# Kernel tuning notes

Hardware: AMD Instinct MI355X
Metric: run time of the kernel (lower is better)

Reference implementation:

```python
import jax, jax.numpy as jnp
import numpy as np

N_NODES = 100000
N_EDGES = 1000000
IN_FEAT = 128
OUT_FEAT = 128
NUM_RELS = 64
NUM_BASES = 16
SUBMAT_IN = IN_FEAT // NUM_BASES   # 8
SUBMAT_OUT = OUT_FEAT // NUM_BASES # 8


def setup_inputs() -> dict:
    key = jax.random.key(0)
    k = jax.random.split(key, 8)
    h = jax.random.normal(k[0], (N_NODES, IN_FEAT), dtype=jnp.float32)
    norm = jax.random.uniform(k[1], (N_EDGES, 1), dtype=jnp.float32)
    src = jax.random.randint(k[2], (N_EDGES,), 0, N_NODES, dtype=jnp.int32)
    dst = jax.random.randint(k[3], (N_EDGES,), 0, N_NODES, dtype=jnp.int32)
    r = jax.random.randint(k[4], (N_EDGES,), 0, NUM_RELS, dtype=jnp.int32)
    # learned params (xavier-uniform style scale)
    wscale = np.sqrt(6.0 / (SUBMAT_IN + SUBMAT_OUT)) * np.sqrt(2.0)
    weight = jax.random.uniform(k[5], (NUM_RELS, NUM_BASES * SUBMAT_IN * SUBMAT_OUT),
                                minval=-wscale, maxval=wscale, dtype=jnp.float32)
    lscale = np.sqrt(6.0 / (IN_FEAT + OUT_FEAT)) * np.sqrt(2.0)
    loop_weight = jax.random.uniform(k[6], (IN_FEAT, OUT_FEAT),
                                     minval=-lscale, maxval=lscale, dtype=jnp.float32)
    h_bias = jnp.zeros((OUT_FEAT,), dtype=jnp.float32)
    return {"h": h, "norm": norm, "weight": weight, "loop_weight": loop_weight,
            "h_bias": h_bias, "src": src, "dst": dst, "r": r}


def reference(h, norm, weight, loop_weight, h_bias, src, dst, r):
    E = src.shape[0]
    # per-edge block-diagonal weights: (E, B, si, so)
    w = weight[r].reshape(E, NUM_BASES, SUBMAT_IN, SUBMAT_OUT)
    # src features split into blocks: (E, B, si)
    hs = h[src].reshape(E, NUM_BASES, SUBMAT_IN)
    # small bmm per block, flatten to (E, OUT_FEAT)
    msg = jnp.einsum('ebi,ebio->ebo', hs, w).reshape(E, OUT_FEAT)
    msg = msg * norm
    # scatter-sum to destination nodes
    agg = jax.ops.segment_sum(msg, dst, num_segments=N_NODES)
    # self-loop message (dropout=0.0) + bias
    out = agg + h_bias + h @ loop_weight
    return jax.nn.relu(out)
```

## Files before the change

kernel.cpp:

```cpp
#include <hip/hip_runtime.h>
#include <stdint.h>

#define N_NODES 100000
#define N_EDGES 1000000
#define IN_F 128
#define OUT_F 128
#define NUM_RELS 64
#define NB_SCAN ((N_NODES + 255) / 256)
#define N_WAVES 16384

typedef _Float16 half2v __attribute__((ext_vector_type(2)));

__device__ __forceinline__ float dot2f(uint32_t hu, uint32_t wu, float acc) {
#if __has_builtin(__builtin_amdgcn_fdot2)
    return __builtin_amdgcn_fdot2(__builtin_bit_cast(half2v, hu),
                                  __builtin_bit_cast(half2v, wu), acc, false);
#else
    half2v a = __builtin_bit_cast(half2v, hu);
    half2v b = __builtin_bit_cast(half2v, wu);
    acc = fmaf((float)a.x, (float)b.x, acc);
    acc = fmaf((float)a.y, (float)b.y, acc);
    return acc;
#endif
}

__device__ __forceinline__ uint32_t pkh2(float x, float y) {
    half2v v;
    v.x = (_Float16)x;
    v.y = (_Float16)y;
    return __builtin_bit_cast(uint32_t, v);
}

__global__ __launch_bounds__(256) void gemm_selfloop(
    const float* __restrict__ h, const float* __restrict__ W,
    const float* __restrict__ bias, float* __restrict__ out, int n_nodes)
{
    const int tid = threadIdx.x;
    const int ty = tid >> 4, tx = tid & 15;
    const int node0 = blockIdx.x * 128 + ty * 8;
    const int o0 = tx * 8;

    float acc[8][8];
#pragma unroll
    for (int j = 0; j < 8; ++j)
#pragma unroll
        for (int i = 0; i < 8; ++i) acc[j][i] = 0.f;

    int nidx[8];
#pragma unroll
    for (int j = 0; j < 8; ++j) {
        int n = node0 + j;
        nidx[j] = n < n_nodes ? n : (n_nodes - 1);
    }

    for (int k = 0; k < IN_F; k += 4) {
        float hsv[8][4];
#pragma unroll
        for (int j = 0; j < 8; ++j) {
            float4 hv = *reinterpret_cast<const float4*>(h + (size_t)nidx[j] * IN_F + k);
            *reinterpret_cast<float4*>(hsv[j]) = hv;
        }
#pragma unroll
        for (int kk = 0; kk < 4; ++kk) {
            const float* wrow = W + (size_t)(k + kk) * OUT_F + o0;
            float wr[8];
            *reinterpret_cast<float4*>(wr)     = *reinterpret_cast<const float4*>(wrow);
            *reinterpret_cast<float4*>(wr + 4) = *reinterpret_cast<const float4*>(wrow + 4);
#pragma unroll
            for (int j = 0; j < 8; ++j) {
                const float hk = hsv[j][kk];
#pragma unroll
                for (int i = 0; i < 8; ++i)
                    acc[j][i] = fmaf(hk, wr[i], acc[j][i]);
            }
        }
    }

    float br[8];
    *reinterpret_cast<float4*>(br)     = *reinterpret_cast<const float4*>(bias + o0);
    *reinterpret_cast<float4*>(br + 4) = *reinterpret_cast<const float4*>(bias + o0 + 4);

#pragma unroll
    for (int j = 0; j < 8; ++j) {
        int n = node0 + j;
        if (n < n_nodes) {
            float4 v0, v1;
            v0.x = acc[j][0] + br[0]; v0.y = acc[j][1] + br[1];
            v0.z = acc[j][2] + br[2]; v0.w = acc[j][3] + br[3];
            v1.x = acc[j][4] + br[4]; v1.y = acc[j][5] + br[5];
            v1.z = acc[j][6] + br[6]; v1.w = acc[j][7] + br[7];
            float* op = out + (size_t)n * OUT_F + o0;
            *reinterpret_cast<float4*>(op)     = v0;
            *reinterpret_cast<float4*>(op + 4) = v1;
        }
    }
}

__global__ __launch_bounds__(256) void prep_hist_h16(
    const float* __restrict__ weight, uint32_t* __restrict__ wsw,
    const int* __restrict__ dst, int* __restrict__ cnt,
    const float* __restrict__ h, uint4* __restrict__ h16_4,
    int n_edges, int do_h16)
{
    int t = blockIdx.x * 256 + threadIdx.x;
    if (t < NUM_RELS * 512) {
        int r    = t >> 9;
        int p    = t & 511;
        int half = p >> 8;
        int w8   = p & 255;
        int l    = w8 >> 2;
        int ip   = w8 & 3;
        int b    = l >> 2;
        int q    = l & 3;
        int o    = 2 * q + half;
        const float* s = weight + (size_t)r * 1024 + b * 64 + (2 * ip) * 8 + o;
        half2v v;
        v.x = (_Float16)s[0];
        v.y = (_Float16)s[8];
        wsw[t] = __builtin_bit_cast(uint32_t, v);
        return;
    }
    int e = t - NUM_RELS * 512;
    if (e < n_edges) {
        atomicAdd(&cnt[dst[e]], 1);
        return;
    }
    if (!do_h16) return;
    int t2 = e - n_edges;
    if (t2 < N_NODES * IN_F / 8) {
        const float4* hp = reinterpret_cast<const float4*>(h + (size_t)t2 * 8);
        float4 a = hp[0], c = hp[1];
        uint4 r;
        r.x = pkh2(a.x, a.y);
        r.y = pkh2(a.z, a.w);
        r.z = pkh2(c.x, c.y);
        r.w = pkh2(c.z, c.w);
        h16_4[t2] = r;
    }
}

__global__ __launch_bounds__(256) void block_sums(
    const int* __restrict__ cnt, int* __restrict__ part, int n)
{
    __shared__ int sdata[256];
    int i = blockIdx.x * 256 + threadIdx.x;
    sdata[threadIdx.x] = (i < n) ? cnt[i] : 0;
    __syncthreads();
    for (int s = 128; s > 0; s >>= 1) {
        if (threadIdx.x < s) sdata[threadIdx.x] += sdata[threadIdx.x + s];
        __syncthreads();
    }
    if (threadIdx.x == 0) part[blockIdx.x] = sdata[0];
}

__global__ __launch_bounds__(256) void write_off2(
    const int* __restrict__ cnt, const int* __restrict__ part,
    int* __restrict__ off, int* __restrict__ cur, int n, int n_edges)
{
    __shared__ int sdata[256];
    __shared__ int buf[256];
    const int tid = threadIdx.x;
    const int bid = blockIdx.x;

    int psum = 0;
    for (int t = tid; t < bid; t += 256) psum += part[t];
    sdata[tid] = psum;
    __syncthreads();
    for (int s = 128; s > 0; s >>= 1) {
        if (tid < s) sdata[tid] += sdata[tid + s];
        __syncthreads();
    }
    const int blockoff = sdata[0];

    int i = bid * 256 + tid;
    int v = (i < n) ? cnt[i] : 0;
    buf[tid] = v;
    __syncthreads();
    for (int ofs = 1; ofs < 256; ofs <<= 1) {
        int t = (tid >= ofs) ? buf[tid - ofs] : 0;
        __syncthreads();
        buf[tid] += t;
        __syncthreads();
    }
    int excl = buf[tid] - v + blockoff;
    if (i < n) { off[i] = excl; cur[i] = excl; }
    if (i == n - 1) off[n] = n_edges;
}

__global__ __launch_bounds__(256) void fill_and_part(
    const int* __restrict__ src, const int* __restrict__ dst,
    const int* __restrict__ rel, const float* __restrict__ norm,
    int* __restrict__ cur, int2* __restrict__ emeta,
    const int* __restrict__ off, int* __restrict__ wstart, int n_edges)
{
    int t = blockIdx.x * 256 + threadIdx.x;
    if (t < n_edges) {
        int d = dst[t];
        int p = atomicAdd(&cur[d], 1);
        int2 m;
        m.x = src[t] | (rel[t] << 20);
        m.y = __float_as_int(norm[t]);
        emeta[p] = m;
    } else {
        int w = t - n_edges;
        if (w <= N_WAVES) {
            if (w == 0) {
                wstart[0] = 0;
            } else if (w == N_WAVES) {
                wstart[N_WAVES] = N_NODES;
            } else {
                int target = (int)(((long long)N_EDGES * w) / N_WAVES);
                int lo = 0, hi = N_NODES - 1;
                while (lo < hi) {
                    int mid = (lo + hi) >> 1;
                    if (off[mid + 1] > target) hi = mid; else lo = mid + 1;
                }
                wstart[w] = lo;
            }
        }
    }
}

__global__ __launch_bounds__(1024, 4) void gather_nodes9(
    const uint4* __restrict__ h16_4, const uint32_t* __restrict__ wsw,
    const int* __restrict__ off, const int2* __restrict__ emeta,
    const int* __restrict__ wstart, float* __restrict__ out)
{
    __shared__ uint32_t wlds[NUM_RELS * 512];

    {
        uint4* l4 = reinterpret_cast<uint4*>(wlds);
        const uint4* g4 = reinterpret_cast<const uint4*>(wsw);
        int t = threadIdx.x;
#pragma unroll
        for (int k = 0; k < 8; ++k)
            l4[t + k * 1024] = g4[t + k * 1024];
    }
    __syncthreads();

    const int lane = threadIdx.x & 63;
    const int wid  = threadIdx.x >> 6;
    const int wv   = blockIdx.x * 16 + wid;
    const int b = lane >> 2;
    const int q = lane & 3;
    const uint32_t lbase = (uint32_t)(lane * 4);

    const int n0 = wstart[wv];
    const int n1 = wstart[wv + 1];
    if (n0 >= n1) return;

    int j = off[n0];
    int e_next = off[n0 + 1];

    int2 m0 = emeta[j];
    int2 m1 = emeta[j + 1];
    int2 m2 = emeta[j + 2];
    uint4 hv0 = h16_4[((uint32_t)m0.x & 0xFFFFFu) * 16 + b];
    uint4 hv1 = h16_4[((uint32_t)m1.x & 0xFFFFFu) * 16 + b];

    uint32_t base0 = ((uint32_t)m0.x >> 20) * 512 + lbase;
    uint4 wa = *reinterpret_cast<const uint4*>(&wlds[base0]);
    uint4 wb = *reinterpret_cast<const uint4*>(&wlds[base0 + 256]);

    for (int d = n0; d < n1; ++d) {
        const int idx2 = (d + 2 < n1) ? d + 2 : n1;
        const int e_nn = off[idx2];
        float a0 = 0.f, a1 = 0.f;

        while (j < e_next) {
            int2 m3 = emeta[j + 3];
            uint4 hv2 = h16_4[((uint32_t)m2.x & 0xFFFFFu) * 16 + b];
            uint32_t bn = ((uint32_t)m1.x >> 20) * 512 + lbase;
            uint4 wna = *reinterpret_cast<const uint4*>(&wlds[bn]);
            uint4 wnb = *reinterpret_cast<const uint4*>(&wlds[bn + 256]);

            float s0 = dot2f(hv0.x, wa.x, 0.f);
            s0 = dot2f(hv0.y, wa.y, s0);
            s0 = dot2f(hv0.z, wa.z, s0);
            s0 = dot2f(hv0.w, wa.w, s0);
            float s1 = dot2f(hv0.x, wb.x, 0.f);
            s1 = dot2f(hv0.y, wb.y, s1);
            s1 = dot2f(hv0.z, wb.z, s1);
            s1 = dot2f(hv0.w, wb.w, s1);

            const float nm = __int_as_float(m0.y);
            a0 = fmaf(s0, nm, a0);
            a1 = fmaf(s1, nm, a1);

            m0 = m1; m1 = m2; m2 = m3;
            hv0 = hv1; hv1 = hv2;
            wa = wna; wb = wnb;
            ++j;
        }

        float2* op = reinterpret_cast<float2*>(out + (size_t)d * OUT_F + b * 8 + 2 * q);
        float2 bse = *op;
        float2 res;
        res.x = fmaxf(bse.x + a0, 0.f);
        res.y = fmaxf(bse.y + a1, 0.f);
        *op = res;

        e_next = e_nn;
    }
}

__global__ __launch_bounds__(1024, 4) void gather_nodes6(
    const float* __restrict__ h, const uint32_t* __restrict__ wsw,
    const int* __restrict__ off, const int2* __restrict__ emeta,
    const int* __restrict__ wstart, float* __restrict__ out)
{
    __shared__ uint32_t wlds[NUM_RELS * 512];
    {
        uint4* l4 = reinterpret_cast<uint4*>(wlds);
        const uint4* g4 = reinterpret_cast<const uint4*>(wsw);
        int t = threadIdx.x;
#pragma unroll
        for (int k = 0; k < 8; ++k)
            l4[t + k * 1024] = g4[t + k * 1024];
    }
    __syncthreads();

    const int lane = threadIdx.x & 63;
    const int wid  = threadIdx.x >> 6;
    const int wv   = blockIdx.x * 16 + wid;
    const int b = lane >> 2;
    const int q = lane & 3;
    const uint32_t lbase = (uint32_t)(lane * 4);

    const int n0 = wstart[wv];
    const int n1 = wstart[wv + 1];
    if (n0 >= n1) return;

    int j = off[n0];
    int2 m0 = emeta[j];
    int2 m1 = emeta[j + 1];
    int2 m2 = emeta[j + 2];

    const float4* hr0 = reinterpret_cast<const float4*>(
        h + (size_t)((uint32_t)m0.x & 0xFFFFFu) * IN_F + b * 8);
    float4 h0A = hr0[0], h0B = hr0[1];
    const float4* hr1 = reinterpret_cast<const float4*>(
        h + (size_t)((uint32_t)m1.x & 0xFFFFFu) * IN_F + b * 8);
    float4 h1A = hr1[0], h1B = hr1[1];

    uint32_t base0 = ((uint32_t)m0.x >> 20) * 512 + lbase;
    uint4 wa = *reinterpret_cast<const uint4*>(&wlds[base0]);
    uint4 wb = *reinterpret_cast<const uint4*>(&wlds[base0 + 256]);

    for (int d = n0; d < n1; ++d) {
        const int end_d = off[d + 1];
        float a0 = 0.f, a1 = 0.f;

        while (j < end_d) {
            int2 m3 = emeta[j + 3];
            const float4* hr2 = reinterpret_cast<const float4*>(
                h + (size_t)((uint32_t)m2.x & 0xFFFFFu) * IN_F + b * 8);
            float4 h2A = hr2[0], h2B = hr2[1];
            uint32_t bn = ((uint32_t)m1.x >> 20) * 512 + lbase;
            uint4 wna = *reinterpret_cast<const uint4*>(&wlds[bn]);
            uint4 wnb = *reinterpret_cast<const uint4*>(&wlds[bn + 256]);

            uint32_t h01 = __builtin_bit_cast(uint32_t, __builtin_amdgcn_cvt_pkrtz(h0A.x, h0A.y));
            uint32_t h23 = __builtin_bit_cast(uint32_t, __builtin_amdgcn_cvt_pkrtz(h0A.z, h0A.w));
            uint32_t h45 = __builtin_bit_cast(uint32_t, __builtin_amdgcn_cvt_pkrtz(h0B.x, h0B.y));
            uint32_t h67 = __builtin_bit_cast(uint32_t, __builtin_amdgcn_cvt_pkrtz(h0B.z, h0B.w));

            float s0 = dot2f(h01, wa.x, 0.f);
            s0 = dot2f(h23, wa.y, s0);
            s0 = dot2f(h45, wa.z, s0);
            s0 = dot2f(h67, wa.w, s0);
            float s1 = dot2f(h01, wb.x, 0.f);
            s1 = dot2f(h23, wb.y, s1);
            s1 = dot2f(h45, wb.z, s1);
            s1 = dot2f(h67, wb.w, s1);

            const float nm = __int_as_float(m0.y);
            a0 = fmaf(s0, nm, a0);
            a1 = fmaf(s1, nm, a1);

            m0 = m1; m1 = m2; m2 = m3;
            h0A = h1A; h0B = h1B; h1A = h2A; h1B = h2B;
            wa = wna; wb = wnb;
            ++j;
        }

        float2* op = reinterpret_cast<float2*>(out + (size_t)d * OUT_F + b * 8 + 2 * q);
        float2 bse = *op;
        float2 res;
        res.x = fmaxf(bse.x + a0, 0.f);
        res.y = fmaxf(bse.y + a1, 0.f);
        *op = res;
    }
}

extern "C" void kernel_launch(void* const* d_in, const int* in_sizes, int n_in,
                              void* d_out, int out_size, void* d_ws, size_t ws_size,
                              hipStream_t stream)
{
    const float* h      = (const float*)d_in[0];
    const float* norm   = (const float*)d_in[1];
    const float* weight = (const float*)d_in[2];
    const float* loop_w = (const float*)d_in[3];
    const float* bias   = (const float*)d_in[4];
    const int*   src    = (const int*)d_in[5];
    const int*   dst    = (const int*)d_in[6];
    const int*   rel    = (const int*)d_in[7];
    float* out = (float*)d_out;

    char* wsb = (char*)d_ws;
    char* ws0 = wsb;
    int*  cnt    = (int*)wsb;  wsb += sizeof(int) * N_NODES;
    int*  off    = (int*)wsb;  wsb += sizeof(int) * (N_NODES + 1);
    int*  cur    = (int*)wsb;  wsb += sizeof(int) * N_NODES;
    int*  part   = (int*)wsb;  wsb += sizeof(int) * 512;
    int*  wstart = (int*)wsb;  wsb += sizeof(int) * (N_WAVES + 1);
    wsb = (char*)(((uintptr_t)wsb + 15) & ~(uintptr_t)15);
    uint32_t* wsw = (uint32_t*)wsb; wsb += sizeof(uint32_t) * NUM_RELS * 512;
    int2* emeta = (int2*)wsb;  wsb += sizeof(int2) * (N_EDGES + 3);
    wsb = (char*)(((uintptr_t)wsb + 15) & ~(uintptr_t)15);
    uint4* h16_4 = (uint4*)wsb; wsb += (size_t)N_NODES * IN_F * 2;

    const int use_h16 = (size_t)(wsb - ws0) <= ws_size;

    hipMemsetAsync(cnt, 0, sizeof(int) * N_NODES, stream);
    hipMemsetAsync(emeta + N_EDGES, 0, 3 * sizeof(int2), stream);

    const int h16_threads = use_h16 ? (N_NODES * IN_F / 8) : 0;
    const int ph_grid = (NUM_RELS * 512 + N_EDGES + h16_threads + 255) / 256;
    prep_hist_h16<<<ph_grid, 256, 0, stream>>>(weight, wsw, dst, cnt,
                                               h, h16_4, N_EDGES, use_h16);
    block_sums<<<NB_SCAN, 256, 0, stream>>>(cnt, part, N_NODES);
    write_off2<<<NB_SCAN, 256, 0, stream>>>(cnt, part, off, cur, N_NODES, N_EDGES);
    const int fp_grid = (N_EDGES + N_WAVES + 1 + 255) / 256;
    fill_and_part<<<fp_grid, 256, 0, stream>>>(src, dst, rel, norm, cur, emeta,
                                               off, wstart, N_EDGES);

    gemm_selfloop<<<(N_NODES + 127) / 128, 256, 0, stream>>>(h, loop_w, bias, out, N_NODES);
    if (use_h16) {
        gather_nodes9<<<1024, 1024, 0, stream>>>(h16_4, wsw, off, emeta, wstart, out);
    } else {
        gather_nodes6<<<1024, 1024, 0, stream>>>(h, wsw, off, emeta, wstart, out);
    }
}
```

Measured before the change: 330.8 us.

## Fuse self-loop GEMM into prep kernel and make gather persistent with fewer blocks

```diff
diff --git a/kernel.cpp b/kernel.cpp
--- a/kernel.cpp
+++ b/kernel.cpp
@@ -8,6 +8,8 @@
 #define NUM_RELS 64
 #define NB_SCAN ((N_NODES + 255) / 256)
 #define N_WAVES 16384
+#define GEMM_B ((N_NODES + 127) / 128)
+#define GATHER_B 256
 
 typedef _Float16 half2v __attribute__((ext_vector_type(2)));
 
@@ -31,78 +33,77 @@
     return __builtin_bit_cast(uint32_t, v);
 }
 
-__global__ __launch_bounds__(256) void gemm_selfloop(
+__global__ __launch_bounds__(256) void prep_gemm_fused(
     const float* __restrict__ h, const float* __restrict__ W,
-    const float* __restrict__ bias, float* __restrict__ out, int n_nodes)
-{
-    const int tid = threadIdx.x;
-    const int ty = tid >> 4, tx = tid & 15;
-    const int node0 = blockIdx.x * 128 + ty * 8;
-    const int o0 = tx * 8;
-
-    float acc[8][8];
-#pragma unroll
-    for (int j = 0; j < 8; ++j)
-#pragma unroll
-        for (int i = 0; i < 8; ++i) acc[j][i] = 0.f;
-
-    int nidx[8];
-#pragma unroll
-    for (int j = 0; j < 8; ++j) {
-        int n = node0 + j;
-        nidx[j] = n < n_nodes ? n : (n_nodes - 1);
-    }
-
-    for (int k = 0; k < IN_F; k += 4) {
-        float hsv[8][4];
-#pragma unroll
-        for (int j = 0; j < 8; ++j) {
-            float4 hv = *reinterpret_cast<const float4*>(h + (size_t)nidx[j] * IN_F + k);
-            *reinterpret_cast<float4*>(hsv[j]) = hv;
-        }
-#pragma unroll
-        for (int kk = 0; kk < 4; ++kk) {
-            const float* wrow = W + (size_t)(k + kk) * OUT_F + o0;
-            float wr[8];
-            *reinterpret_cast<float4*>(wr)     = *reinterpret_cast<const float4*>(wrow);
-            *reinterpret_cast<float4*>(wr + 4) = *reinterpret_cast<const float4*>(wrow + 4);
-#pragma unroll
-            for (int j = 0; j < 8; ++j) {
-                const float hk = hsv[j][kk];
-#pragma unroll
-                for (int i = 0; i < 8; ++i)
-                    acc[j][i] = fmaf(hk, wr[i], acc[j][i]);
-            }
-        }
-    }
-
-    float br[8];
-    *reinterpret_cast<float4*>(br)     = *reinterpret_cast<const float4*>(bias + o0);
-    *reinterpret_cast<float4*>(br + 4) = *reinterpret_cast<const float4*>(bias + o0 + 4);
-
-#pragma unroll
-    for (int j = 0; j < 8; ++j) {
-        int n = node0 + j;
-        if (n < n_nodes) {
-            float4 v0, v1;
-            v0.x = acc[j][0] + br[0]; v0.y = acc[j][1] + br[1];
-            v0.z = acc[j][2] + br[2]; v0.w = acc[j][3] + br[3];
-            v1.x = acc[j][4] + br[4]; v1.y = acc[j][5] + br[5];
-            v1.z = acc[j][6] + br[6]; v1.w = acc[j][7] + br[7];
-            float* op = out + (size_t)n * OUT_F + o0;
-            *reinterpret_cast<float4*>(op)     = v0;
-            *reinterpret_cast<float4*>(op + 4) = v1;
-        }
-    }
-}
-
-__global__ __launch_bounds__(256) void prep_hist_h16(
+    const float* __restrict__ bias, float* __restrict__ out,
     const float* __restrict__ weight, uint32_t* __restrict__ wsw,
     const int* __restrict__ dst, int* __restrict__ cnt,
-    const float* __restrict__ h, uint4* __restrict__ h16_4,
-    int n_edges, int do_h16)
-{
-    int t = blockIdx.x * 256 + threadIdx.x;
+    uint4* __restrict__ h16_4, int n_edges, int do_h16)
+{
+    if (blockIdx.x < GEMM_B) {
+        const int tid = threadIdx.x;
+        const int ty = tid >> 4, tx = tid & 15;
+        const int node0 = blockIdx.x * 128 + ty * 8;
+        const int o0 = tx * 8;
+
+        float acc[8][8];
+#pragma unroll
+        for (int j = 0; j < 8; ++j)
+#pragma unroll
+            for (int i = 0; i < 8; ++i) acc[j][i] = 0.f;
+
+        int nidx[8];
+#pragma unroll
+        for (int j = 0; j < 8; ++j) {
+            int n = node0 + j;
+            nidx[j] = n < N_NODES ? n : (N_NODES - 1);
+        }
+
+        for (int k = 0; k < IN_F; k += 4) {
+            float hsv[8][4];
+#pragma unroll
+            for (int j = 0; j < 8; ++j) {
+                float4 hv = *reinterpret_cast<const float4*>(h + (size_t)nidx[j] * IN_F + k);
+                *reinterpret_cast<float4*>(hsv[j]) = hv;
+            }
+#pragma unroll
+            for (int kk = 0; kk < 4; ++kk) {
+                const float* wrow = W + (size_t)(k + kk) * OUT_F + o0;
+                float wr[8];
+                *reinterpret_cast<float4*>(wr)     = *reinterpret_cast<const float4*>(wrow);
+                *reinterpret_cast<float4*>(wr + 4) = *reinterpret_cast<const float4*>(wrow + 4);
+#pragma unroll
+                for (int j = 0; j < 8; ++j) {
+                    const float hk = hsv[j][kk];
+#pragma unroll
+                    for (int i = 0; i < 8; ++i)
+                        acc[j][i] = fmaf(hk, wr[i], acc[j][i]);
+                }
+            }
+        }
+
+        float br[8];
+        *reinterpret_cast<float4*>(br)     = *reinterpret_cast<const float4*>(bias + o0);
+        *reinterpret_cast<float4*>(br + 4) = *reinterpret_cast<const float4*>(bias + o0 + 4);
+
+#pragma unroll
+        for (int j = 0; j < 8; ++j) {
+            int n = node0 + j;
+            if (n < N_NODES) {
+                float4 v0, v1;
+                v0.x = acc[j][0] + br[0]; v0.y = acc[j][1] + br[1];
+                v0.z = acc[j][2] + br[2]; v0.w = acc[j][3] + br[3];
+                v1.x = acc[j][4] + br[4]; v1.y = acc[j][5] + br[5];
+                v1.z = acc[j][6] + br[6]; v1.w = acc[j][7] + br[7];
+                float* op = out + (size_t)n * OUT_F + o0;
+                *reinterpret_cast<float4*>(op)     = v0;
+                *reinterpret_cast<float4*>(op + 4) = v1;
+            }
+        }
+        return;
+    }
+
+    int t = (blockIdx.x - GEMM_B) * 256 + threadIdx.x;
     if (t < NUM_RELS * 512) {
         int r    = t >> 9;
         int p    = t & 511;
@@ -217,11 +218,14 @@
                 }
                 wstart[w] = lo;
             }
-        }
-    }
-}
-
-__global__ __launch_bounds__(1024, 4) void gather_nodes9(
+        } else if (w <= N_WAVES + 3) {
+            int2 z; z.x = 0; z.y = 0;
+            emeta[n_edges + (w - N_WAVES - 1)] = z;
+        }
+    }
+}
+
+__global__ __launch_bounds__(1024, 4) void gather_nodes10(
     const uint4* __restrict__ h16_4, const uint32_t* __restrict__ wsw,
     const int* __restrict__ off, const int2* __restrict__ emeta,
     const int* __restrict__ wstart, float* __restrict__ out)
@@ -240,67 +244,68 @@
 
     const int lane = threadIdx.x & 63;
     const int wid  = threadIdx.x >> 6;
-    const int wv   = blockIdx.x * 16 + wid;
     const int b = lane >> 2;
     const int q = lane & 3;
     const uint32_t lbase = (uint32_t)(lane * 4);
 
-    const int n0 = wstart[wv];
-    const int n1 = wstart[wv + 1];
-    if (n0 >= n1) return;
-
-    int j = off[n0];
-    int e_next = off[n0 + 1];
-
-    int2 m0 = emeta[j];
-    int2 m1 = emeta[j + 1];
-    int2 m2 = emeta[j + 2];
-    uint4 hv0 = h16_4[((uint32_t)m0.x & 0xFFFFFu) * 16 + b];
-    uint4 hv1 = h16_4[((uint32_t)m1.x & 0xFFFFFu) * 16 + b];
-
-    uint32_t base0 = ((uint32_t)m0.x >> 20) * 512 + lbase;
-    uint4 wa = *reinterpret_cast<const uint4*>(&wlds[base0]);
-    uint4 wb = *reinterpret_cast<const uint4*>(&wlds[base0 + 256]);
-
-    for (int d = n0; d < n1; ++d) {
-        const int idx2 = (d + 2 < n1) ? d + 2 : n1;
-        const int e_nn = off[idx2];
-        float a0 = 0.f, a1 = 0.f;
-
-        while (j < e_next) {
-            int2 m3 = emeta[j + 3];
-            uint4 hv2 = h16_4[((uint32_t)m2.x & 0xFFFFFu) * 16 + b];
-            uint32_t bn = ((uint32_t)m1.x >> 20) * 512 + lbase;
-            uint4 wna = *reinterpret_cast<const uint4*>(&wlds[bn]);
-            uint4 wnb = *reinterpret_cast<const uint4*>(&wlds[bn + 256]);
-
-            float s0 = dot2f(hv0.x, wa.x, 0.f);
-            s0 = dot2f(hv0.y, wa.y, s0);
-            s0 = dot2f(hv0.z, wa.z, s0);
-            s0 = dot2f(hv0.w, wa.w, s0);
-            float s1 = dot2f(hv0.x, wb.x, 0.f);
-            s1 = dot2f(hv0.y, wb.y, s1);
-            s1 = dot2f(hv0.z, wb.z, s1);
-            s1 = dot2f(hv0.w, wb.w, s1);
-
-            const float nm = __int_as_float(m0.y);
-            a0 = fmaf(s0, nm, a0);
-            a1 = fmaf(s1, nm, a1);
-
-            m0 = m1; m1 = m2; m2 = m3;
-            hv0 = hv1; hv1 = hv2;
-            wa = wna; wb = wnb;
-            ++j;
-        }
-
-        float2* op = reinterpret_cast<float2*>(out + (size_t)d * OUT_F + b * 8 + 2 * q);
-        float2 bse = *op;
-        float2 res;
-        res.x = fmaxf(bse.x + a0, 0.f);
-        res.y = fmaxf(bse.y + a1, 0.f);
-        *op = res;
-
-        e_next = e_nn;
+    for (int wv = blockIdx.x * 16 + wid; wv < N_WAVES; wv += GATHER_B * 16) {
+        const int n0 = wstart[wv];
+        const int n1 = wstart[wv + 1];
+        if (n0 >= n1) continue;
+
+        int j = off[n0];
+        int e_next = off[n0 + 1];
+
+        int2 m0 = emeta[j];
+        int2 m1 = emeta[j + 1];
+        int2 m2 = emeta[j + 2];
+        uint4 hv0 = h16_4[((uint32_t)m0.x & 0xFFFFFu) * 16 + b];
+        uint4 hv1 = h16_4[((uint32_t)m1.x & 0xFFFFFu) * 16 + b];
+
+        uint32_t base0 = ((uint32_t)m0.x >> 20) * 512 + lbase;
+        uint4 wa = *reinterpret_cast<const uint4*>(&wlds[base0]);
+        uint4 wb = *reinterpret_cast<const uint4*>(&wlds[base0 + 256]);
+
+        for (int d = n0; d < n1; ++d) {
+            const int idx2 = (d + 2 < n1) ? d + 2 : n1;
+            const int e_nn = off[idx2];
+            float a0 = 0.f, a1 = 0.f;
+
+            while (j < e_next) {
+                int2 m3 = emeta[j + 3];
+                uint4 hv2 = h16_4[((uint32_t)m2.x & 0xFFFFFu) * 16 + b];
+                uint32_t bn = ((uint32_t)m1.x >> 20) * 512 + lbase;
+                uint4 wna = *reinterpret_cast<const uint4*>(&wlds[bn]);
+                uint4 wnb = *reinterpret_cast<const uint4*>(&wlds[bn + 256]);
+
+                float s0 = dot2f(hv0.x, wa.x, 0.f);
+                s0 = dot2f(hv0.y, wa.y, s0);
+                s0 = dot2f(hv0.z, wa.z, s0);
+                s0 = dot2f(hv0.w, wa.w, s0);
+                float s1 = dot2f(hv0.x, wb.x, 0.f);
+                s1 = dot2f(hv0.y, wb.y, s1);
+                s1 = dot2f(hv0.z, wb.z, s1);
+                s1 = dot2f(hv0.w, wb.w, s1);
+
+                const float nm = __int_as_float(m0.y);
+                a0 = fmaf(s0, nm, a0);
+                a1 = fmaf(s1, nm, a1);
+
+                m0 = m1; m1 = m2; m2 = m3;
+                hv0 = hv1; hv1 = hv2;
+                wa = wna; wb = wnb;
+                ++j;
+            }
+
+            float2* op = reinterpret_cast<float2*>(out + (size_t)d * OUT_F + b * 8 + 2 * q);
+            float2 bse = *op;
+            float2 res;
+            res.x = fmaxf(bse.x + a0, 0.f);
+            res.y = fmaxf(bse.y + a1, 0.f);
+            *op = res;
+
+            e_next = e_nn;
+        }
     }
 }
 
@@ -322,74 +327,75 @@
 
     const int lane = threadIdx.x & 63;
     const int wid  = threadIdx.x >> 6;
-    const int wv   = blockIdx.x * 16 + wid;
     const int b = lane >> 2;
     const int q = lane & 3;
     const uint32_t lbase = (uint32_t)(lane * 4);
 
-    const int n0 = wstart[wv];
-    const int n1 = wstart[wv + 1];
-    if (n0 >= n1) return;
-
-    int j = off[n0];
-    int2 m0 = emeta[j];
-    int2 m1 = emeta[j + 1];
-    int2 m2 = emeta[j + 2];
-
-    const float4* hr0 = reinterpret_cast<const float4*>(
-        h + (size_t)((uint32_t)m0.x & 0xFFFFFu) * IN_F + b * 8);
-    float4 h0A = hr0[0], h0B = hr0[1];
-    const float4* hr1 = reinterpret_cast<const float4*>(
-        h + (size_t)((uint32_t)m1.x & 0xFFFFFu) * IN_F + b * 8);
-    float4 h1A = hr1[0], h1B = hr1[1];
-
-    uint32_t base0 = ((uint32_t)m0.x >> 20) * 512 + lbase;
-    uint4 wa = *reinterpret_cast<const uint4*>(&wlds[base0]);
-    uint4 wb = *reinterpret_cast<const uint4*>(&wlds[base0 + 256]);
-
-    for (int d = n0; d < n1; ++d) {
-        const int end_d = off[d + 1];
-        float a0 = 0.f, a1 = 0.f;
-
-        while (j < end_d) {
-            int2 m3 = emeta[j + 3];
-            const float4* hr2 = reinterpret_cast<const float4*>(
-                h + (size_t)((uint32_t)m2.x & 0xFFFFFu) * IN_F + b * 8);
-            float4 h2A = hr2[0], h2B = hr2[1];
-            uint32_t bn = ((uint32_t)m1.x >> 20) * 512 + lbase;
-            uint4 wna = *reinterpret_cast<const uint4*>(&wlds[bn]);
-            uint4 wnb = *reinterpret_cast<const uint4*>(&wlds[bn + 256]);
-
-            uint32_t h01 = __builtin_bit_cast(uint32_t, __builtin_amdgcn_cvt_pkrtz(h0A.x, h0A.y));
-            uint32_t h23 = __builtin_bit_cast(uint32_t, __builtin_amdgcn_cvt_pkrtz(h0A.z, h0A.w));
-            uint32_t h45 = __builtin_bit_cast(uint32_t, __builtin_amdgcn_cvt_pkrtz(h0B.x, h0B.y));
-            uint32_t h67 = __builtin_bit_cast(uint32_t, __builtin_amdgcn_cvt_pkrtz(h0B.z, h0B.w));
-
-            float s0 = dot2f(h01, wa.x, 0.f);
-            s0 = dot2f(h23, wa.y, s0);
-            s0 = dot2f(h45, wa.z, s0);
-            s0 = dot2f(h67, wa.w, s0);
-            float s1 = dot2f(h01, wb.x, 0.f);
-            s1 = dot2f(h23, wb.y, s1);
-            s1 = dot2f(h45, wb.z, s1);
-            s1 = dot2f(h67, wb.w, s1);
-
-            const float nm = __int_as_float(m0.y);
-            a0 = fmaf(s0, nm, a0);
-            a1 = fmaf(s1, nm, a1);
-
-            m0 = m1; m1 = m2; m2 = m3;
-            h0A = h1A; h0B = h1B; h1A = h2A; h1B = h2B;
-            wa = wna; wb = wnb;
-            ++j;
-        }
-
-        float2* op = reinterpret_cast<float2*>(out + (size_t)d * OUT_F + b * 8 + 2 * q);
-        float2 bse = *op;
-        float2 res;
-        res.x = fmaxf(bse.x + a0, 0.f);
-        res.y = fmaxf(bse.y + a1, 0.f);
-        *op = res;
+    for (int wv = blockIdx.x * 16 + wid; wv < N_WAVES; wv += GATHER_B * 16) {
+        const int n0 = wstart[wv];
+        const int n1 = wstart[wv + 1];
+        if (n0 >= n1) continue;
+
+        int j = off[n0];
+        int2 m0 = emeta[j];
+        int2 m1 = emeta[j + 1];
+        int2 m2 = emeta[j + 2];
+
+        const float4* hr0 = reinterpret_cast<const float4*>(
+            h + (size_t)((uint32_t)m0.x & 0xFFFFFu) * IN_F + b * 8);
+        float4 h0A = hr0[0], h0B = hr0[1];
+        const float4* hr1 = reinterpret_cast<const float4*>(
+            h + (size_t)((uint32_t)m1.x & 0xFFFFFu) * IN_F + b * 8);
+        float4 h1A = hr1[0], h1B = hr1[1];
+
+        uint32_t base0 = ((uint32_t)m0.x >> 20) * 512 + lbase;
+        uint4 wa = *reinterpret_cast<const uint4*>(&wlds[base0]);
+        uint4 wb = *reinterpret_cast<const uint4*>(&wlds[base0 + 256]);
+
+        for (int d = n0; d < n1; ++d) {
+            const int end_d = off[d + 1];
+            float a0 = 0.f, a1 = 0.f;
+
+            while (j < end_d) {
+                int2 m3 = emeta[j + 3];
+                const float4* hr2 = reinterpret_cast<const float4*>(
+                    h + (size_t)((uint32_t)m2.x & 0xFFFFFu) * IN_F + b * 8);
+                float4 h2A = hr2[0], h2B = hr2[1];
+                uint32_t bn = ((uint32_t)m1.x >> 20) * 512 + lbase;
+                uint4 wna = *reinterpret_cast<const uint4*>(&wlds[bn]);
+                uint4 wnb = *reinterpret_cast<const uint4*>(&wlds[bn + 256]);
+
+                uint32_t h01 = __builtin_bit_cast(uint32_t, __builtin_amdgcn_cvt_pkrtz(h0A.x, h0A.y));
+                uint32_t h23 = __builtin_bit_cast(uint32_t, __builtin_amdgcn_cvt_pkrtz(h0A.z, h0A.w));
+                uint32_t h45 = __builtin_bit_cast(uint32_t, __builtin_amdgcn_cvt_pkrtz(h0B.x, h0B.y));
+                uint32_t h67 = __builtin_bit_cast(uint32_t, __builtin_amdgcn_cvt_pkrtz(h0B.z, h0B.w));
+
+                float s0 = dot2f(h01, wa.x, 0.f);
+                s0 = dot2f(h23, wa.y, s0);
+                s0 = dot2f(h45, wa.z, s0);
+                s0 = dot2f(h67, wa.w, s0);
+                float s1 = dot2f(h01, wb.x, 0.f);
+                s1 = dot2f(h23, wb.y, s1);
+                s1 = dot2f(h45, wb.z, s1);
+                s1 = dot2f(h67, wb.w, s1);
+
+                const float nm = __int_as_float(m0.y);
+                a0 = fmaf(s0, nm, a0);
+                a1 = fmaf(s1, nm, a1);
+
+                m0 = m1; m1 = m2; m2 = m3;
+                h0A = h1A; h0B = h1B; h1A = h2A; h1B = h2B;
+                wa = wna; wb = wnb;
+                ++j;
+            }
+
+            float2* op = reinterpret_cast<float2*>(out + (size_t)d * OUT_F + b * 8 + 2 * q);
+            float2 bse = *op;
+            float2 res;
+            res.x = fmaxf(bse.x + a0, 0.f);
+            res.y = fmaxf(bse.y + a1, 0.f);
+            *op = res;
+        }
     }
 }
 
@@ -423,22 +429,20 @@
     const int use_h16 = (size_t)(wsb - ws0) <= ws_size;
 
     hipMemsetAsync(cnt, 0, sizeof(int) * N_NODES, stream);
-    hipMemsetAsync(emeta + N_EDGES, 0, 3 * sizeof(int2), stream);
 
     const int h16_threads = use_h16 ? (N_NODES * IN_F / 8) : 0;
-    const int ph_grid = (NUM_RELS * 512 + N_EDGES + h16_threads + 255) / 256;
-    prep_hist_h16<<<ph_grid, 256, 0, stream>>>(weight, wsw, dst, cnt,
-                                               h, h16_4, N_EDGES, use_h16);
+    const int prep_blocks = (NUM_RELS * 512 + N_EDGES + h16_threads + 255) / 256;
+    prep_gemm_fused<<<GEMM_B + prep_blocks, 256, 0, stream>>>(
+        h, loop_w, bias, out, weight, wsw, dst, cnt, h16_4, N_EDGES, use_h16);
     block_sums<<<NB_SCAN, 256, 0, stream>>>(cnt, part, N_NODES);
     write_off2<<<NB_SCAN, 256, 0, stream>>>(cnt, part, off, cur, N_NODES, N_EDGES);
-    const int fp_grid = (N_EDGES + N_WAVES + 1 + 255) / 256;
+    const int fp_grid = (N_EDGES + N_WAVES + 4 + 255) / 256;
     fill_and_part<<<fp_grid, 256, 0, stream>>>(src, dst, rel, norm, cur, emeta,
                                                off, wstart, N_EDGES);
 
-    gemm_selfloop<<<(N_NODES + 127) / 128, 256, 0, stream>>>(h, loop_w, bias, out, N_NODES);
     if (use_h16) {
-        gather_nodes9<<<1024, 1024, 0, stream>>>(h16_4, wsw, off, emeta, wstart, out);
+        gather_nodes10<<<GATHER_B, 1024, 0, stream>>>(h16_4, wsw, off, emeta, wstart, out);
     } else {
-        gather_nodes6<<<1024, 1024, 0, stream>>>(h, wsw, off, emeta, wstart, out);
-    }
-}
+        gather_nodes6<<<GATHER_B, 1024, 0, stream>>>(h, wsw, off, emeta, wstart, out);
+    }
+}
```

Result: faster. 309.5 us (-6.4%).
